# Kernel tuning notes

Hardware: AMD Instinct MI355X
Metric: run time of the kernel (lower is better)

The kernel has to match this reference:

```python
import jax, jax.numpy as jnp
from jax import lax
import numpy as np

KS = 7       # kernel_size
STRIDE = 2
PAD = KS // 2  # -inf padding (morphological identity) => out = ceil(H/stride)


def _parabolic_kernel(t):
    # z_i = linspace(-ks//2 + 1, ks//2, ks) -> centered offsets, e.g. [-3..3] for ks=7
    z_i = jnp.linspace(-(KS // 2), KS // 2, KS, dtype=jnp.float32)
    z_c = z_i[:, None] ** 2 + z_i[None, :] ** 2      # (KS, KS)
    # identical across channels (repeat_interleave of the same 2D kernel)
    return -z_c / (4.0 * t)


def setup_inputs() -> dict:
    key = jax.random.key(0)
    k1, k2 = jax.random.split(key)
    f = jax.random.normal(k1, (16, 128, 256, 256), dtype=jnp.float32)
    t = jnp.asarray(0.5, dtype=jnp.float32)
    return {"f": f, "t": t}


def reference(f, t):
    # Max-plus (morphological dilation) pooling with learned parabolic structuring element:
    # out[b,c,i,j] = max_{u,v} f[b,c, i*s + u - PAD, j*s + v - PAD] + h[u,v]
    B, C, H, W = f.shape
    h = _parabolic_kernel(t)                         # (KS, KS)
    Ho = (H + 2 * PAD - KS) // STRIDE + 1
    Wo = (W + 2 * PAD - KS) // STRIDE + 1
    neg_inf = jnp.asarray(-jnp.inf, f.dtype)
    fp = jnp.pad(f, ((0, 0), (0, 0), (PAD, PAD), (PAD, PAD)), constant_values=neg_inf)
    out = jnp.full((B, C, Ho, Wo), neg_inf, dtype=f.dtype)
    for u in range(KS):          # small fixed KS*KS loop; each iter is a strided slice + fused max
        for v in range(KS):
            win = lax.slice(
                fp,
                (0, 0, u, v),
                (B, C, u + STRIDE * (Ho - 1) + 1, v + STRIDE * (Wo - 1) + 1),
                (1, 1, STRIDE, STRIDE),
            )  # (B, C, Ho, Wo)
            out = jnp.maximum(out, win + h[u, v])
    return out
```

## Files before the change

### kernel.cpp

```cpp
#include <hip/hip_runtime.h>


#define KS 7
#define PAD 3
#define H 256
#define W 256
#define HO 128
#define WO 128
#define TH 32
#define TW 32
#define ROWS 69
#define COLS 72
#define SSTRIDE 76
#define GSTRIDE 36

__global__ __launch_bounds__(256)
void pp_kernel(const float* __restrict__ f, const float* __restrict__ tptr,
               float* __restrict__ out) {
    __shared__ float sin_[ROWS * SSTRIDE];
    __shared__ float g_[ROWS * GSTRIDE];

    const int tid   = threadIdx.x;
    const int blk   = blockIdx.x;
    const int tile  = blk & 15;
    const int plane = blk >> 4;
    const int i0 = (tile >> 2) * TH;
    const int j0 = (tile & 3) * TW;

    const float tv = tptr[0];
    float hu[KS];
#pragma unroll
    for (int v = 0; v < KS; ++v) {
        const float z = (float)(v - PAD);
        hu[v] = -(z * z) / (4.0f * tv);
    }

    const int gy0 = 2 * i0 - 3;
    const int gx0 = 2 * j0 - 4;
    const float* fplane = f + (size_t)plane * (H * W);
    const float NEG = -__builtin_inff();

#pragma unroll 1
    for (int idx = tid; idx < ROWS * (COLS / 4); idx += 256) {
        const int r  = idx / (COLS / 4);
        const int c4 = idx - r * (COLS / 4);
        const int gy = gy0 + r;
        const int gx = gx0 + 4 * c4;
        float4 val;
        if (gy >= 0 && gy < H && gx >= 0 && gx < W) {
            val = *(const float4*)(fplane + gy * W + gx);
        } else {
            val = make_float4(NEG, NEG, NEG, NEG);
        }
        *(float4*)(&sin_[r * SSTRIDE + 4 * c4]) = val;
    }
    __syncthreads();

    {
        const int q  = tid & 7;
        const int yb = tid >> 3;
        const int jr = q * 4;
#pragma unroll 1
        for (int y = yb; y < ROWS; y += 32) {
            const float* row = &sin_[y * SSTRIDE + 2 * jr];
            const float4 w0 = *(const float4*)(row);
            const float4 w1 = *(const float4*)(row + 4);
            const float4 w2 = *(const float4*)(row + 8);
            const float4 w3 = *(const float4*)(row + 12);
            const float s[16] = {w0.x, w0.y, w0.z, w0.w, w1.x, w1.y, w1.z, w1.w,
                                 w2.x, w2.y, w2.z, w2.w, w3.x, w3.y, w3.z, w3.w};
            float4 gv;
            float* gp = (float*)&gv;
#pragma unroll
            for (int jj = 0; jj < 4; ++jj) {
                float m = s[2 * jj + 1] + hu[0];
#pragma unroll
                for (int v = 1; v < KS; ++v)
                    m = fmaxf(m, s[2 * jj + 1 + v] + hu[v]);
                gp[jj] = m;
            }
            *(float4*)(&g_[y * GSTRIDE + jr]) = gv;
        }
    }
    __syncthreads();

    {
        const int j  = tid & 31;
        const int ir = (tid >> 5) * 4;
        float col[13];
#pragma unroll
        for (int k = 0; k < 13; ++k)
            col[k] = g_[(2 * ir + k) * GSTRIDE + j];
        float* oplane = out + (size_t)plane * (HO * WO);
#pragma unroll
        for (int ii = 0; ii < 4; ++ii) {
            float m = col[2 * ii] + hu[0];
#pragma unroll
            for (int u = 1; u < KS; ++u)
                m = fmaxf(m, col[2 * ii + u] + hu[u]);
            oplane[(size_t)(i0 + ir + ii) * WO + (j0 + j)] = m;
        }
    }
}

extern "C" void kernel_launch(void* const* d_in, const int* in_sizes, int n_in,
                              void* d_out, int out_size, void* d_ws, size_t ws_size,
                              hipStream_t stream) {
    const float* f = (const float*)d_in[0];
    const float* t = (const float*)d_in[1];
    float* out = (float*)d_out;
    pp_kernel<<<dim3(2048 * 16), dim3(256), 0, stream>>>(f, t, out);
}
```

Measured before the change: 729.2 us.

## Halve tile height, hoist global loads before setup, remap block order

Tile height drops from 32 to 16 output rows, so the grid doubles and each block needs a smaller shared-memory footprint. The launch bound now asks for 8 blocks per CU to raise occupancy. All global float4 loads are issued up front with clamped addresses and predicated stores, so memory latency overlaps the kernel-coefficient setup. Block IDs are remapped so that concurrently resident blocks are spread across planes, changing DRAM access locality. The cost is more halo rereads per output, since row overlap grows relative to tile height, plus extra register pressure from the staged loads.

```diff
diff --git a/kernel.cpp b/kernel.cpp
--- a/kernel.cpp
+++ b/kernel.cpp
@@ -7,25 +7,51 @@
 #define W 256
 #define HO 128
 #define WO 128
-#define TH 32
+#define TH 16
 #define TW 32
-#define ROWS 69
+#define ROWS 37
+#define NF4 18
 #define COLS 72
 #define SSTRIDE 76
 #define GSTRIDE 36
+#define NITEMS (ROWS * NF4)
 
-__global__ __launch_bounds__(256)
+__global__ __launch_bounds__(256, 8)
 void pp_kernel(const float* __restrict__ f, const float* __restrict__ tptr,
                float* __restrict__ out) {
-    __shared__ float sin_[ROWS * SSTRIDE];
-    __shared__ float g_[ROWS * GSTRIDE];
+    __shared__ __align__(16) float sin_[ROWS * SSTRIDE];
+    __shared__ __align__(16) float g_[ROWS * GSTRIDE];
 
-    const int tid   = threadIdx.x;
-    const int blk   = blockIdx.x;
-    const int tile  = blk & 15;
-    const int plane = blk >> 4;
-    const int i0 = (tile >> 2) * TH;
-    const int j0 = (tile & 3) * TW;
+    const int tid = threadIdx.x;
+    const int bid = blockIdx.x;
+    const int lid   = (bid & 7) * 8192 + (bid >> 3);
+    const int plane = lid >> 5;
+    const int t5    = lid & 31;
+    const int i0    = (t5 & 7) * TH;
+    const int j0    = (t5 >> 3) * TW;
+
+    const int gy0 = 2 * i0 - 3;
+    const int gx0 = 2 * j0 - 4;
+    const float* __restrict__ fplane = f + (size_t)plane * (H * W);
+    const float NEG = -__builtin_inff();
+
+    float4 raw[3];
+    int lofs[3];
+    bool keep[3], inb[3];
+#pragma unroll
+    for (int k = 0; k < 3; ++k) {
+        const int idx = tid + 256 * k;
+        const int r   = idx / NF4;
+        const int c4  = idx - r * NF4;
+        const int gy  = gy0 + r;
+        const int gx  = gx0 + 4 * c4;
+        keep[k] = (idx < NITEMS);
+        inb[k]  = keep[k] & (gy >= 0) & (gy < H) & (gx >= 0) & (gx < W);
+        const int cy = min(max(gy, 0), H - 1);
+        const int cx = min(max(gx, 0), W - 4);
+        raw[k]  = *(const float4*)(fplane + cy * W + cx);
+        lofs[k] = r * SSTRIDE + 4 * c4;
+    }
 
     const float tv = tptr[0];
     float hu[KS];
@@ -35,24 +61,12 @@
         hu[v] = -(z * z) / (4.0f * tv);
     }
 
-    const int gy0 = 2 * i0 - 3;
-    const int gx0 = 2 * j0 - 4;
-    const float* fplane = f + (size_t)plane * (H * W);
-    const float NEG = -__builtin_inff();
-
-#pragma unroll 1
-    for (int idx = tid; idx < ROWS * (COLS / 4); idx += 256) {
-        const int r  = idx / (COLS / 4);
-        const int c4 = idx - r * (COLS / 4);
-        const int gy = gy0 + r;
-        const int gx = gx0 + 4 * c4;
-        float4 val;
-        if (gy >= 0 && gy < H && gx >= 0 && gx < W) {
-            val = *(const float4*)(fplane + gy * W + gx);
-        } else {
-            val = make_float4(NEG, NEG, NEG, NEG);
+#pragma unroll
+    for (int k = 0; k < 3; ++k) {
+        if (keep[k]) {
+            float4 val = inb[k] ? raw[k] : make_float4(NEG, NEG, NEG, NEG);
+            *(float4*)(&sin_[lofs[k]]) = val;
         }
-        *(float4*)(&sin_[r * SSTRIDE + 4 * c4]) = val;
     }
     __syncthreads();
 
@@ -86,20 +100,21 @@
 
     {
         const int j  = tid & 31;
-        const int ir = (tid >> 5) * 4;
-        float col[13];
+        const int ir = (tid >> 5) * 2;
+        float col[9];
 #pragma unroll
-        for (int k = 0; k < 13; ++k)
+        for (int k = 0; k < 9; ++k)
             col[k] = g_[(2 * ir + k) * GSTRIDE + j];
-        float* oplane = out + (size_t)plane * (HO * WO);
+        float m0 = col[0] + hu[0];
+        float m1 = col[2] + hu[0];
 #pragma unroll
-        for (int ii = 0; ii < 4; ++ii) {
-            float m = col[2 * ii] + hu[0];
-#pragma unroll
-            for (int u = 1; u < KS; ++u)
-                m = fmaxf(m, col[2 * ii + u] + hu[u]);
-            oplane[(size_t)(i0 + ir + ii) * WO + (j0 + j)] = m;
+        for (int u = 1; u < KS; ++u) {
+            m0 = fmaxf(m0, col[u]     + hu[u]);
+            m1 = fmaxf(m1, col[u + 2] + hu[u]);
         }
+        float* __restrict__ oplane = out + (size_t)plane * (HO * WO);
+        oplane[(size_t)(i0 + ir)     * WO + (j0 + j)] = m0;
+        oplane[(size_t)(i0 + ir + 1) * WO + (j0 + j)] = m1;
     }
 }
 
@@ -109,5 +124,5 @@
     const float* f = (const float*)d_in[0];
     const float* t = (const float*)d_in[1];
     float* out = (float*)d_out;
-    pp_kernel<<<dim3(2048 * 16), dim3(256), 0, stream>>>(f, t, out);
+    pp_kernel<<<dim3(2048 * 32), dim3(256), 0, stream>>>(f, t, out);
 }
```

Measured after the change: 705.3 us. 3.3% less time.

## Restructure pooling into full-width row strips with vertical pass in registers

Applied to the files above, without the earlier changes.

Replaces 32x32 output tiles with full-width 16-row strips per block. The vertical 7-tap max is computed directly from global float4 loads in registers, with symmetric tap pairing, and only the vertical result is staged in shared memory. The horizontal pass then reads that staged buffer and writes float4 outputs. This removes one shared-memory round trip and one barrier, cuts the horizontal halo reloads, and adds a block-index swizzle. In exchange, each thread loads 9 overlapping rows from global memory (overlap between row pairs relies on cache), and occupancy depends on the 512-thread launch bounds.

```diff
diff --git a/kernel.cpp b/kernel.cpp
--- a/kernel.cpp
+++ b/kernel.cpp
@@ -1,105 +1,110 @@
 #include <hip/hip_runtime.h>
 
 
-#define KS 7
-#define PAD 3
 #define H 256
 #define W 256
 #define HO 128
 #define WO 128
-#define TH 32
-#define TW 32
-#define ROWS 69
-#define COLS 72
-#define SSTRIDE 76
-#define GSTRIDE 36
+#define TH 16
+#define VPAD 4
+#define VSTRIDE 276
 
-__global__ __launch_bounds__(256)
+__device__ __forceinline__ float4 f4max(float4 a, float4 b) {
+    return make_float4(fmaxf(a.x, b.x), fmaxf(a.y, b.y), fmaxf(a.z, b.z), fmaxf(a.w, b.w));
+}
+__device__ __forceinline__ float4 f4adds(float4 a, float s) {
+    return make_float4(a.x + s, a.y + s, a.z + s, a.w + s);
+}
+
+__global__ __launch_bounds__(512, 6)
 void pp_kernel(const float* __restrict__ f, const float* __restrict__ tptr,
                float* __restrict__ out) {
-    __shared__ float sin_[ROWS * SSTRIDE];
-    __shared__ float g_[ROWS * GSTRIDE];
+    __shared__ __align__(16) float v_[TH * VSTRIDE];
 
-    const int tid   = threadIdx.x;
-    const int blk   = blockIdx.x;
-    const int tile  = blk & 15;
-    const int plane = blk >> 4;
-    const int i0 = (tile >> 2) * TH;
-    const int j0 = (tile & 3) * TW;
+    const int tid = threadIdx.x;
+    const int bid = blockIdx.x;
+    const int lid   = (bid & 7) * 2048 + (bid >> 3);
+    const int plane = lid >> 3;
+    const int strip = lid & 7;
+    const int i0    = strip * TH;
 
-    const float tv = tptr[0];
-    float hu[KS];
-#pragma unroll
-    for (int v = 0; v < KS; ++v) {
-        const float z = (float)(v - PAD);
-        hu[v] = -(z * z) / (4.0f * tv);
+    const float tv  = tptr[0];
+    const float inv = 1.0f / (4.0f * tv);
+    const float h0 = -9.0f * inv, h1 = -4.0f * inv, h2 = -1.0f * inv;
+    const float NEG = -__builtin_inff();
+
+    const float* __restrict__ fplane = f + (size_t)plane * (H * W);
+
+    if (tid < 32) {
+        const int r   = tid & 15;
+        const int off = (tid < 16) ? 0 : (VPAD + W);
+        *(float4*)(&v_[r * VSTRIDE + off]) = make_float4(NEG, NEG, NEG, NEG);
     }
 
-    const int gy0 = 2 * i0 - 3;
-    const int gx0 = 2 * j0 - 4;
-    const float* fplane = f + (size_t)plane * (H * W);
-    const float NEG = -__builtin_inff();
+    {
+        const int x4    = (tid & 63) * 4;
+        const int ipair = tid >> 6;
+        const int ib    = 2 * ipair;
+        const int gy0   = 2 * (i0 + ib) - 3;
 
-#pragma unroll 1
-    for (int idx = tid; idx < ROWS * (COLS / 4); idx += 256) {
-        const int r  = idx / (COLS / 4);
-        const int c4 = idx - r * (COLS / 4);
-        const int gy = gy0 + r;
-        const int gx = gx0 + 4 * c4;
-        float4 val;
-        if (gy >= 0 && gy < H && gx >= 0 && gx < W) {
-            val = *(const float4*)(fplane + gy * W + gx);
+        float4 r[9];
+#pragma unroll
+        for (int k = 0; k < 9; ++k) {
+            const int cy = min(max(gy0 + k, 0), H - 1);
+            r[k] = *(const float4*)(fplane + cy * W + x4);
+        }
+
+        float4 vA, vB;
+        if (gy0 >= 0 && gy0 + 8 <= H - 1) {
+            vA = f4max(f4max(f4adds(f4max(r[0], r[6]), h0),
+                             f4adds(f4max(r[1], r[5]), h1)),
+                       f4max(f4adds(f4max(r[2], r[4]), h2), r[3]));
+            vB = f4max(f4max(f4adds(f4max(r[2], r[8]), h0),
+                             f4adds(f4max(r[3], r[7]), h1)),
+                       f4max(f4adds(f4max(r[4], r[6]), h2), r[5]));
         } else {
-            val = make_float4(NEG, NEG, NEG, NEG);
+            const float hu[7] = {h0, h1, h2, 0.0f, h2, h1, h0};
+            float4 a = make_float4(NEG, NEG, NEG, NEG);
+            float4 b = make_float4(NEG, NEG, NEG, NEG);
+#pragma unroll
+            for (int u = 0; u < 7; ++u) {
+                const int gyA = gy0 + u;
+                const int gyB = gy0 + 2 + u;
+                const float hA = (gyA >= 0 && gyA < H) ? hu[u] : NEG;
+                const float hB = (gyB >= 0 && gyB < H) ? hu[u] : NEG;
+                a = f4max(a, f4adds(r[u], hA));
+                b = f4max(b, f4adds(r[u + 2], hB));
+            }
+            vA = a; vB = b;
         }
-        *(float4*)(&sin_[r * SSTRIDE + 4 * c4]) = val;
+
+        *(float4*)(&v_[(ib)     * VSTRIDE + VPAD + x4]) = vA;
+        *(float4*)(&v_[(ib + 1) * VSTRIDE + VPAD + x4]) = vB;
     }
     __syncthreads();
 
     {
-        const int q  = tid & 7;
-        const int yb = tid >> 3;
-        const int jr = q * 4;
-#pragma unroll 1
-        for (int y = yb; y < ROWS; y += 32) {
-            const float* row = &sin_[y * SSTRIDE + 2 * jr];
-            const float4 w0 = *(const float4*)(row);
-            const float4 w1 = *(const float4*)(row + 4);
-            const float4 w2 = *(const float4*)(row + 8);
-            const float4 w3 = *(const float4*)(row + 12);
-            const float s[16] = {w0.x, w0.y, w0.z, w0.w, w1.x, w1.y, w1.z, w1.w,
-                                 w2.x, w2.y, w2.z, w2.w, w3.x, w3.y, w3.z, w3.w};
-            float4 gv;
-            float* gp = (float*)&gv;
+        const int i  = tid >> 5;
+        const int jg = tid & 31;
+        const int c0 = 4 * jg;
+        const float* p = &v_[i * VSTRIDE + 2 * c0];
+        const float4 a = *(const float4*)(p);
+        const float4 b = *(const float4*)(p + 4);
+        const float4 c = *(const float4*)(p + 8);
+        const float4 d = *(const float4*)(p + 12);
+        const float s[16] = {a.x, a.y, a.z, a.w, b.x, b.y, b.z, b.w,
+                             c.x, c.y, c.z, c.w, d.x, d.y, d.z, d.w};
+        float4 o;
+        float* op = (float*)&o;
 #pragma unroll
-            for (int jj = 0; jj < 4; ++jj) {
-                float m = s[2 * jj + 1] + hu[0];
-#pragma unroll
-                for (int v = 1; v < KS; ++v)
-                    m = fmaxf(m, s[2 * jj + 1 + v] + hu[v]);
-                gp[jj] = m;
-            }
-            *(float4*)(&g_[y * GSTRIDE + jr]) = gv;
+        for (int dd = 0; dd < 4; ++dd) {
+            const float m0 = fmaxf(s[2 * dd + 1], s[2 * dd + 7]) + h0;
+            const float m1 = fmaxf(s[2 * dd + 2], s[2 * dd + 6]) + h1;
+            const float m2 = fmaxf(s[2 * dd + 3], s[2 * dd + 5]) + h2;
+            op[dd] = fmaxf(fmaxf(m0, m1), fmaxf(m2, s[2 * dd + 4]));
         }
-    }
-    __syncthreads();
-
-    {
-        const int j  = tid & 31;
-        const int ir = (tid >> 5) * 4;
-        float col[13];
-#pragma unroll
-        for (int k = 0; k < 13; ++k)
-            col[k] = g_[(2 * ir + k) * GSTRIDE + j];
-        float* oplane = out + (size_t)plane * (HO * WO);
-#pragma unroll
-        for (int ii = 0; ii < 4; ++ii) {
-            float m = col[2 * ii] + hu[0];
-#pragma unroll
-            for (int u = 1; u < KS; ++u)
-                m = fmaxf(m, col[2 * ii + u] + hu[u]);
-            oplane[(size_t)(i0 + ir + ii) * WO + (j0 + j)] = m;
-        }
+        float* __restrict__ orow = out + (size_t)plane * (HO * WO) + (size_t)(i0 + i) * WO;
+        *(float4*)(orow + c0) = o;
     }
 }
 
@@ -109,5 +114,5 @@
     const float* f = (const float*)d_in[0];
     const float* t = (const float*)d_in[1];
     float* out = (float*)d_out;
-    pp_kernel<<<dim3(2048 * 16), dim3(256), 0, stream>>>(f, t, out);
+    pp_kernel<<<dim3(2048 * 8), dim3(512), 0, stream>>>(f, t, out);
 }
```

Measured after the change: 710.7 us. 2.5% less time.
